# Kernel tuning notes

Measured on AMD Instinct MI355X. Metric: run time of the kernel, lower is better.

## Reference

```python
import jax, jax.numpy as jnp
import numpy as np

D_MODEL = 1024
NHEAD = 16
D_K = D_MODEL // NHEAD


def setup_inputs() -> dict:
    key = jax.random.key(0)
    ks = jax.random.split(key, 8)
    B, S, D = 4, 2048, D_MODEL
    scale = 1.0 / np.sqrt(D)  # rough xavier-like scale for weights
    return {
        "query": jax.random.normal(ks[0], (B, S, D), jnp.float32),
        "key_": jax.random.normal(ks[1], (B, S, D), jnp.float32),
        "value": jax.random.normal(ks[2], (B, S, D), jnp.float32),
        "w_q": jax.random.normal(ks[3], (D, D), jnp.float32) * scale,
        "w_k": jax.random.normal(ks[4], (D, D), jnp.float32) * scale,
        "w_v": jax.random.normal(ks[5], (D, D), jnp.float32) * scale,
        "w_o": jax.random.normal(ks[6], (D, D), jnp.float32) * scale,
        "b_o": jnp.zeros((D,), jnp.float32),
    }


def reference(query, key_, value, w_q, w_k, w_v, w_o, b_o):
    B, S, D = query.shape
    H, dk = NHEAD, D_K
    # torch Linear: x @ W.T ; reshape to [B, H, S, dk]
    def split_heads(x, w):
        return (x @ w.T).reshape(B, S, H, dk).transpose(0, 2, 1, 3)

    Q = split_heads(query, w_q)
    K = split_heads(key_, w_k)
    V = split_heads(value, w_v)

    scores = jnp.einsum("bhqd,bhkd->bhqk", Q, K) / jnp.sqrt(jnp.float32(dk))
    attn = jax.nn.softmax(scores, axis=-1)  # [B,H,S,S]
    ctx = jnp.einsum("bhqk,bhkd->bhqd", attn, V)
    ctx = ctx.transpose(0, 2, 1, 3).reshape(B, S, D)
    out = ctx @ w_o.T + b_o
    return out
```

## Files before the change

kernel.cpp:

```cpp
#include <hip/hip_runtime.h>
#include <hip/hip_bf16.h>
#include <stdint.h>

#define D_MODEL 1024
#define NHEAD   16
#define DK      64
#define BATCH   4
#define SEQ     2048
#define MROWS   (BATCH*SEQ)

typedef __hip_bfloat16 bf16;
typedef __attribute__((ext_vector_type(8))) short short8;
typedef __attribute__((ext_vector_type(4))) float f32x4;
typedef __attribute__((ext_vector_type(4))) unsigned int uint4t;

typedef __attribute__((address_space(1))) unsigned int as1_uint;
typedef __attribute__((address_space(3))) unsigned int as3_uint;

#define MFMA32(a,b,c) __builtin_amdgcn_mfma_f32_16x16x32_bf16((a),(b),(c),0,0,0)

static __device__ __forceinline__ void load_lds16(const bf16* g, bf16* l) {
  __builtin_amdgcn_global_load_lds((const as1_uint*)g, (as3_uint*)l, 16, 0, 0);
}

static __device__ __forceinline__ unsigned short bfbits(float x) {
  __hip_bfloat16 h = __float2bfloat16(x);
  return __builtin_bit_cast(unsigned short, h);
}

static __device__ __forceinline__ unsigned int pack2(float lo, float hi) {
  return (unsigned int)bfbits(lo) | ((unsigned int)bfbits(hi) << 16);
}

static __device__ __forceinline__ unsigned int pack2t(float lo, float hi) {
  return (__builtin_bit_cast(unsigned int, lo) >> 16) |
         (__builtin_bit_cast(unsigned int, hi) & 0xffff0000u);
}

__global__ __launch_bounds__(256) void cast_w(const float* __restrict__ i0,
                                              const float* __restrict__ i1,
                                              const float* __restrict__ i2,
                                              const float* __restrict__ i3,
                                              bf16* o0, bf16* o1, bf16* o2, bf16* o3,
                                              float s1) {
  const int z = blockIdx.z;
  const float* in = z == 0 ? i0 : (z == 1 ? i1 : (z == 2 ? i2 : i3));
  bf16* out = z == 0 ? o0 : (z == 1 ? o1 : (z == 2 ? o2 : o3));
  const float s = (z == 1) ? s1 : 1.0f;
  int i = blockIdx.x * 256 + threadIdx.x;
  const float4* p = (const float4*)in;
  float4 a = p[2 * (size_t)i];
  float4 b = p[2 * (size_t)i + 1];
  uint4t u;
  u.x = pack2(a.x * s, a.y * s);
  u.y = pack2(a.z * s, a.w * s);
  u.z = pack2(b.x * s, b.y * s);
  u.w = pack2(b.z * s, b.w * s);
  *(uint4t*)(out + (size_t)i * 8) = u;
}

__global__ __launch_bounds__(256) void cast_x(const float* __restrict__ i0,
                                              const float* __restrict__ i1,
                                              const float* __restrict__ i2,
                                              bf16* o0, bf16* o1, bf16* o2) {
  const int z = blockIdx.z;
  const float* in = z == 0 ? i0 : (z == 1 ? i1 : i2);
  bf16* out = z == 0 ? o0 : (z == 1 ? o1 : o2);
  int i = blockIdx.x * 256 + threadIdx.x;
  const float4* p = (const float4*)in;
  float4 a = p[2 * (size_t)i];
  float4 b = p[2 * (size_t)i + 1];
  uint4t u;
  u.x = pack2(a.x, a.y);
  u.y = pack2(a.z, a.w);
  u.z = pack2(b.x, b.y);
  u.w = pack2(b.z, b.w);
  *(uint4t*)(out + (size_t)i * 8) = u;
}

#define GEMM_STAGE(BUFOFF, KT) do {                                   \
    load_lds16(Ag0 + (KT), As + (BUFOFF) + w * 512);                  \
    load_lds16(Ag1 + (KT), As + (BUFOFF) + 2048 + w * 512);           \
    load_lds16(Bg0 + (KT), Bs + (BUFOFF) + w * 512);                  \
    load_lds16(Bg1 + (KT), Bs + (BUFOFF) + 2048 + w * 512);           \
  } while (0)

#define GEMM_COMPUTE(BUFOFF) do {                                              \
    short8 af[4], bf_[4];                                                      \
    _Pragma("unroll") for (int i = 0; i < 4; ++i) {                            \
      af[i]  = *(const short8*)(As + (BUFOFF) + (wm + i * 16 + lm) * 32 + lq * 8); \
      bf_[i] = *(const short8*)(Bs + (BUFOFF) + (wn + i * 16 + lm) * 32 + lq * 8); \
    }                                                                          \
    _Pragma("unroll") for (int i = 0; i < 4; ++i)                              \
      _Pragma("unroll") for (int j = 0; j < 4; ++j)                            \
        acc[i][j] = MFMA32(af[i], bf_[j], acc[i][j]);                          \
  } while (0)

#define VMCNT0_BAR() do {                                   \
    asm volatile("s_waitcnt vmcnt(0)" ::: "memory");        \
    __syncthreads();                                        \
  } while (0)

__global__ __launch_bounds__(256) void gemm_proj(const bf16* __restrict__ A0,
                                                 const bf16* __restrict__ A1,
                                                 const bf16* __restrict__ A2,
                                                 const bf16* __restrict__ B0,
                                                 const bf16* __restrict__ B1,
                                                 const bf16* __restrict__ B2,
                                                 bf16* C0, bf16* C1, bf16* C2) {
  const int z = blockIdx.z;
  const bf16* A = z == 0 ? A0 : (z == 1 ? A1 : A2);
  const bf16* B = z == 0 ? B0 : (z == 1 ? B1 : B2);
  bf16* C = z == 0 ? C0 : (z == 1 ? C1 : C2);
  const int M = MROWS, N = D_MODEL, K = D_MODEL;

  __shared__ bf16 As[2 * 128 * 32];
  __shared__ bf16 Bs[2 * 128 * 32];
  const int t = threadIdx.x;
  const int w = t >> 6;
  const int lane = t & 63;
  const int lm = lane & 15;
  const int lq = lane >> 4;
  const int wm = (w >> 1) * 64;
  const int wn = (w & 1) * 64;
  const long rowA = (long)blockIdx.x * 128;
  const long rowB = (long)blockIdx.y * 128;

  const int srow = t >> 2;
  const int scol = (t & 3) * 8;
  const bf16* Ag0 = A + (rowA + srow) * K + scol;
  const bf16* Ag1 = A + (rowA + 64 + srow) * K + scol;
  const bf16* Bg0 = B + (rowB + srow) * K + scol;
  const bf16* Bg1 = B + (rowB + 64 + srow) * K + scol;

  const f32x4 fzero = {0.f, 0.f, 0.f, 0.f};
  f32x4 acc[4][4];
#pragma unroll
  for (int i = 0; i < 4; ++i)
#pragma unroll
    for (int j = 0; j < 4; ++j) acc[i][j] = fzero;

  GEMM_STAGE(0, 0);
  VMCNT0_BAR();
  for (int kt = 0; kt < K; kt += 64) {
    if (kt + 32 < K) GEMM_STAGE(4096, kt + 32);
    GEMM_COMPUTE(0);
    VMCNT0_BAR();
    if (kt + 64 < K) GEMM_STAGE(0, kt + 64);
    GEMM_COMPUTE(4096);
    VMCNT0_BAR();
  }

  if (z < 2) {
#pragma unroll
    for (int i = 0; i < 4; ++i) {
      long r0 = rowA + wm + i * 16 + lq * 4;
#pragma unroll
      for (int j = 0; j < 4; ++j) {
        long c = rowB + wn + j * 16 + lm;
#pragma unroll
        for (int r = 0; r < 4; ++r)
          C[(r0 + r) * N + c] = __float2bfloat16(acc[i][j][r]);
      }
    }
  } else {
#pragma unroll
    for (int j = 0; j < 4; ++j) {
      long c = rowB + wn + j * 16 + lm;
#pragma unroll
      for (int i = 0; i < 4; ++i) {
        long r0 = rowA + wm + i * 16 + lq * 4;
        long sp = (r0 & ~63L) | (((r0 >> 5) & 1) * 32) | ((r0 & 15) * 2) | ((r0 >> 4) & 1);
#pragma unroll
        for (int r = 0; r < 4; ++r)
          C[c * M + sp + r * 2] = __float2bfloat16(acc[i][j][r]);
      }
    }
  }
}

__global__ __launch_bounds__(256) void gemm_out(const bf16* __restrict__ A,
                                                const bf16* __restrict__ B,
                                                float* __restrict__ C,
                                                const float* __restrict__ bias) {
  const int M = MROWS, N = D_MODEL, K = D_MODEL;
  __shared__ bf16 As[2 * 128 * 32];
  __shared__ bf16 Bs[2 * 128 * 32];
  const int t = threadIdx.x;
  const int w = t >> 6;
  const int lane = t & 63;
  const int lm = lane & 15;
  const int lq = lane >> 4;
  const int wm = (w >> 1) * 64;
  const int wn = (w & 1) * 64;
  const long rowA = (long)blockIdx.x * 128;
  const long rowB = (long)blockIdx.y * 128;

  const int srow = t >> 2;
  const int scol = (t & 3) * 8;
  const bf16* Ag0 = A + (rowA + srow) * K + scol;
  const bf16* Ag1 = A + (rowA + 64 + srow) * K + scol;
  const bf16* Bg0 = B + (rowB + srow) * K + scol;
  const bf16* Bg1 = B + (rowB + 64 + srow) * K + scol;

  const f32x4 fzero = {0.f, 0.f, 0.f, 0.f};
  f32x4 acc[4][4];
#pragma unroll
  for (int i = 0; i < 4; ++i)
#pragma unroll
    for (int j = 0; j < 4; ++j) acc[i][j] = fzero;

  GEMM_STAGE(0, 0);
  VMCNT0_BAR();
  for (int kt = 0; kt < K; kt += 64) {
    if (kt + 32 < K) GEMM_STAGE(4096, kt + 32);
    GEMM_COMPUTE(0);
    VMCNT0_BAR();
    if (kt + 64 < K) GEMM_STAGE(0, kt + 64);
    GEMM_COMPUTE(4096);
    VMCNT0_BAR();
  }

#pragma unroll
  for (int j = 0; j < 4; ++j) {
    long c = rowB + wn + j * 16 + lm;
    float bz = bias[c];
#pragma unroll
    for (int i = 0; i < 4; ++i) {
      long r0 = rowA + wm + i * 16 + lq * 4;
#pragma unroll
      for (int r = 0; r < 4; ++r)
        C[(r0 + r) * N + c] = acc[i][j][r] + bz;
    }
  }
}

__global__ __launch_bounds__(256, 4) void attn_kernel(const bf16* __restrict__ Qb,
                                                      const bf16* __restrict__ Kb,
                                                      const bf16* __restrict__ Vt,
                                                      bf16* __restrict__ ctx) {
  __shared__ bf16 Ks[64 * 64];
  __shared__ bf16 Vs[64 * 64];
  const int t = threadIdx.x;
  const int w = t >> 6;
  const int lane = t & 63;
  const int lm = lane & 15;
  const int lq = lane >> 4;
  const int bh = blockIdx.x;
  const int b = bh >> 4;
  const int h = bh & 15;
  const int q0 = blockIdx.y * 128 + w * 32;

  const bf16* Qh = Qb + (long)b * SEQ * D_MODEL + h * DK;
  const bf16* Kh = Kb + (long)b * SEQ * D_MODEL + h * DK;
  const bf16* Vh = Vt + (long)h * DK * MROWS + (long)b * SEQ;

  const int sr = lane >> 3;
  const int sc = ((lane & 7) ^ sr) * 8;
  const bf16* kg0 = Kh + (long)(w * 8 + sr) * D_MODEL + sc;
  const bf16* kg1 = Kh + (long)(32 + w * 8 + sr) * D_MODEL + sc;
  const bf16* vg0 = Vh + (long)(w * 8 + sr) * MROWS + sc;
  const bf16* vg1 = Vh + (long)(32 + w * 8 + sr) * MROWS + sc;
  bf16* lk0 = Ks + w * 512;
  bf16* lk1 = Ks + 2048 + w * 512;
  bf16* lv0 = Vs + w * 512;
  bf16* lv1 = Vs + 2048 + w * 512;

  short8 qf[2][2];
#pragma unroll
  for (int qt = 0; qt < 2; ++qt)
#pragma unroll
    for (int ks = 0; ks < 2; ++ks)
      qf[qt][ks] = *(const short8*)(Qh + (long)(q0 + qt * 16 + lm) * D_MODEL + ks * 32 + lq * 8);

  uint4t uo;
  uo.x = 0x3F803F80u; uo.y = 0x3F803F80u; uo.z = 0x3F803F80u; uo.w = 0x3F803F80u;
  const short8 ones8 = __builtin_bit_cast(short8, uo);

  const f32x4 fzero = {0.f, 0.f, 0.f, 0.f};
  f32x4 O[2][4];
  f32x4 lsum[2];
#pragma unroll
  for (int qt = 0; qt < 2; ++qt) {
    lsum[qt] = fzero;
#pragma unroll
    for (int dt = 0; dt < 4; ++dt) O[qt][dt] = fzero;
  }

  const int xs = lm & 7;

  for (int kv = 0; kv < SEQ; kv += 64) {
    load_lds16(kg0, lk0);
    load_lds16(kg1, lk1);
    load_lds16(vg0, lv0);
    load_lds16(vg1, lv1);
    kg0 += 64 * D_MODEL; kg1 += 64 * D_MODEL;
    vg0 += 64; vg1 += 64;
    asm volatile("s_waitcnt vmcnt(0)" ::: "memory");
    __syncthreads();

    short8 kf[4][2];
#pragma unroll
    for (int c = 0; c < 4; ++c)
#pragma unroll
      for (int ks = 0; ks < 2; ++ks)
        kf[c][ks] = *(const short8*)(Ks + (c * 16 + lm) * 64 + (((ks * 4 + lq) ^ xs) * 8));
    short8 vf[4][2];
#pragma unroll
    for (int dt = 0; dt < 4; ++dt)
#pragma unroll
      for (int tt = 0; tt < 2; ++tt)
        vf[dt][tt] = *(const short8*)(Vs + (dt * 16 + lm) * 64 + (((tt * 4 + lq) ^ xs) * 8));

#pragma unroll
    for (int qt = 0; qt < 2; ++qt) {
      f32x4 st[4];
#pragma unroll
      for (int c = 0; c < 4; ++c)
        st[c] = MFMA32(kf[c][0], qf[qt][0], fzero);
#pragma unroll
      for (int c = 0; c < 4; ++c)
        st[c] = MFMA32(kf[c][1], qf[qt][1], st[c]);

      float pe[4][4];
#pragma unroll
      for (int c = 0; c < 4; ++c)
#pragma unroll
        for (int r = 0; r < 4; ++r)
          pe[c][r] = __builtin_amdgcn_exp2f(st[c][r]);

      short8 pf8[2];
#pragma unroll
      for (int tt = 0; tt < 2; ++tt) {
        uint4t u;
        u.x = pack2t(pe[2 * tt][0], pe[2 * tt + 1][0]);
        u.y = pack2t(pe[2 * tt][1], pe[2 * tt + 1][1]);
        u.z = pack2t(pe[2 * tt][2], pe[2 * tt + 1][2]);
        u.w = pack2t(pe[2 * tt][3], pe[2 * tt + 1][3]);
        pf8[tt] = __builtin_bit_cast(short8, u);
      }

#pragma unroll
      for (int tt = 0; tt < 2; ++tt) {
        lsum[qt] = MFMA32(pf8[tt], ones8, lsum[qt]);
#pragma unroll
        for (int dt = 0; dt < 4; ++dt)
          O[qt][dt] = MFMA32(pf8[tt], vf[dt][tt], O[qt][dt]);
      }
    }
    __syncthreads();
  }

#pragma unroll
  for (int qt = 0; qt < 2; ++qt) {
    f32x4 linv;
#pragma unroll
    for (int r = 0; r < 4; ++r) linv[r] = 1.f / lsum[qt][r];
#pragma unroll
    for (int r = 0; r < 4; ++r) {
      long qrow = (long)b * SEQ + q0 + qt * 16 + lq * 4 + r;
#pragma unroll
      for (int dt = 0; dt < 4; ++dt)
        ctx[qrow * D_MODEL + h * DK + dt * 16 + lm] =
            __float2bfloat16(O[qt][dt][r] * linv[r]);
    }
  }
}

extern "C" void kernel_launch(void* const* d_in, const int* in_sizes, int n_in,
                              void* d_out, int out_size, void* d_ws, size_t ws_size,
                              hipStream_t stream) {
  const float* q  = (const float*)d_in[0];
  const float* k  = (const float*)d_in[1];
  const float* v  = (const float*)d_in[2];
  const float* wq = (const float*)d_in[3];
  const float* wk = (const float*)d_in[4];
  const float* wv = (const float*)d_in[5];
  const float* wo = (const float*)d_in[6];
  const float* bo = (const float*)d_in[7];

  char* ws = (char*)d_ws;
  const size_t SZW = (size_t)D_MODEL * D_MODEL * sizeof(bf16);
  const size_t SZX = (size_t)MROWS * D_MODEL * sizeof(bf16);
  bf16* Wq = (bf16*)(ws + 0 * SZW);
  bf16* Wk = (bf16*)(ws + 1 * SZW);
  bf16* Wv = (bf16*)(ws + 2 * SZW);
  bf16* Wo = (bf16*)(ws + 3 * SZW);
  bf16* Xq = (bf16*)(ws + 4 * SZW + 0 * SZX);
  bf16* Xk = (bf16*)(ws + 4 * SZW + 1 * SZX);
  bf16* Xv = (bf16*)(ws + 4 * SZW + 2 * SZX);
  bf16* Qb = (bf16*)(ws + 4 * SZW + 3 * SZX);
  bf16* Kb = (bf16*)(ws + 4 * SZW + 4 * SZX);
  bf16* Vt = Xq;
  bf16* Cx = Xk;

  const float SCL = 0.18033688011112042f;
  const int NW8 = D_MODEL * D_MODEL / 8;
  const int NX8 = MROWS * D_MODEL / 8;

  cast_w<<<dim3(NW8 / 256, 1, 4), 256, 0, stream>>>(wq, wk, wv, wo, Wq, Wk, Wv, Wo, SCL);
  cast_x<<<dim3(NX8 / 256, 1, 3), 256, 0, stream>>>(q, k, v, Xq, Xk, Xv);

  gemm_proj<<<dim3(MROWS / 128, D_MODEL / 128, 3), 256, 0, stream>>>(
      Xq, Xk, Xv, Wq, Wk, Wv, Qb, Kb, Vt);

  attn_kernel<<<dim3(BATCH * NHEAD, SEQ / 128), 256, 0, stream>>>(Qb, Kb, Vt, Cx);

  gemm_out<<<dim3(MROWS / 128, D_MODEL / 128), 256, 0, stream>>>(Cx, Wo, (float*)d_out, bo);
}
```

Measured before the change: 326.4 us.

## Fuse fp32-to-bf16 input cast into projection GEMM and double-buffer attention K/V

```diff
diff --git a/kernel.cpp b/kernel.cpp
--- a/kernel.cpp
+++ b/kernel.cpp
@@ -30,6 +30,12 @@
 
 static __device__ __forceinline__ unsigned int pack2(float lo, float hi) {
   return (unsigned int)bfbits(lo) | ((unsigned int)bfbits(hi) << 16);
+}
+
+static __device__ __forceinline__ unsigned int cvtpk(float lo, float hi) {
+  unsigned int d;
+  asm("v_cvt_pk_bf16_f32 %0, %1, %2" : "=v"(d) : "v"(lo), "v"(hi));
+  return d;
 }
 
 static __device__ __forceinline__ unsigned int pack2t(float lo, float hi) {
@@ -59,25 +65,6 @@
   *(uint4t*)(out + (size_t)i * 8) = u;
 }
 
-__global__ __launch_bounds__(256) void cast_x(const float* __restrict__ i0,
-                                              const float* __restrict__ i1,
-                                              const float* __restrict__ i2,
-                                              bf16* o0, bf16* o1, bf16* o2) {
-  const int z = blockIdx.z;
-  const float* in = z == 0 ? i0 : (z == 1 ? i1 : i2);
-  bf16* out = z == 0 ? o0 : (z == 1 ? o1 : o2);
-  int i = blockIdx.x * 256 + threadIdx.x;
-  const float4* p = (const float4*)in;
-  float4 a = p[2 * (size_t)i];
-  float4 b = p[2 * (size_t)i + 1];
-  uint4t u;
-  u.x = pack2(a.x, a.y);
-  u.y = pack2(a.z, a.w);
-  u.z = pack2(b.x, b.y);
-  u.w = pack2(b.z, b.w);
-  *(uint4t*)(out + (size_t)i * 8) = u;
-}
-
 #define GEMM_STAGE(BUFOFF, KT) do {                                   \
     load_lds16(Ag0 + (KT), As + (BUFOFF) + w * 512);                  \
     load_lds16(Ag1 + (KT), As + (BUFOFF) + 2048 + w * 512);           \
@@ -101,15 +88,37 @@
     __syncthreads();                                        \
   } while (0)
 
-__global__ __launch_bounds__(256) void gemm_proj(const bf16* __restrict__ A0,
-                                                 const bf16* __restrict__ A1,
-                                                 const bf16* __restrict__ A2,
+#define PROJ_LOADA(KT) do {                                  \
+    ar0 = *(const float4*)(Af0 + (KT));                      \
+    ar1 = *(const float4*)(Af0 + (KT) + 4);                  \
+    ar2 = *(const float4*)(Af1 + (KT));                      \
+    ar3 = *(const float4*)(Af1 + (KT) + 4);                  \
+  } while (0)
+
+#define PROJ_STOREA(BUFOFF) do {                             \
+    uint4t u0, u1;                                           \
+    u0.x = cvtpk(ar0.x, ar0.y); u0.y = cvtpk(ar0.z, ar0.w);  \
+    u0.z = cvtpk(ar1.x, ar1.y); u0.w = cvtpk(ar1.z, ar1.w);  \
+    u1.x = cvtpk(ar2.x, ar2.y); u1.y = cvtpk(ar2.z, ar2.w);  \
+    u1.z = cvtpk(ar3.x, ar3.y); u1.w = cvtpk(ar3.z, ar3.w);  \
+    *(uint4t*)(As + (BUFOFF) + t * 8) = u0;                  \
+    *(uint4t*)(As + (BUFOFF) + 2048 + t * 8) = u1;           \
+  } while (0)
+
+#define PROJ_STAGEB(BUFOFF, KT) do {                                  \
+    load_lds16(Bg0 + (KT), Bs + (BUFOFF) + w * 512);                  \
+    load_lds16(Bg1 + (KT), Bs + (BUFOFF) + 2048 + w * 512);           \
+  } while (0)
+
+__global__ __launch_bounds__(256) void gemm_proj(const float* __restrict__ A0,
+                                                 const float* __restrict__ A1,
+                                                 const float* __restrict__ A2,
                                                  const bf16* __restrict__ B0,
                                                  const bf16* __restrict__ B1,
                                                  const bf16* __restrict__ B2,
                                                  bf16* C0, bf16* C1, bf16* C2) {
   const int z = blockIdx.z;
-  const bf16* A = z == 0 ? A0 : (z == 1 ? A1 : A2);
+  const float* A = z == 0 ? A0 : (z == 1 ? A1 : A2);
   const bf16* B = z == 0 ? B0 : (z == 1 ? B1 : B2);
   bf16* C = z == 0 ? C0 : (z == 1 ? C1 : C2);
   const int M = MROWS, N = D_MODEL, K = D_MODEL;
@@ -128,11 +137,13 @@
 
   const int srow = t >> 2;
   const int scol = (t & 3) * 8;
-  const bf16* Ag0 = A + (rowA + srow) * K + scol;
-  const bf16* Ag1 = A + (rowA + 64 + srow) * K + scol;
+  const float* Af0 = A + (rowA + srow) * K + scol;
+  const float* Af1 = A + (rowA + 64 + srow) * K + scol;
   const bf16* Bg0 = B + (rowB + srow) * K + scol;
   const bf16* Bg1 = B + (rowB + 64 + srow) * K + scol;
 
+  float4 ar0, ar1, ar2, ar3;
+
   const f32x4 fzero = {0.f, 0.f, 0.f, 0.f};
   f32x4 acc[4][4];
 #pragma unroll
@@ -140,15 +151,21 @@
 #pragma unroll
     for (int j = 0; j < 4; ++j) acc[i][j] = fzero;
 
-  GEMM_STAGE(0, 0);
+  PROJ_LOADA(0);
+  PROJ_STAGEB(0, 0);
+  PROJ_STOREA(0);
   VMCNT0_BAR();
   for (int kt = 0; kt < K; kt += 64) {
-    if (kt + 32 < K) GEMM_STAGE(4096, kt + 32);
+    if (kt + 32 < K) { PROJ_LOADA(kt + 32); PROJ_STAGEB(4096, kt + 32); }
     GEMM_COMPUTE(0);
-    VMCNT0_BAR();
-    if (kt + 64 < K) GEMM_STAGE(0, kt + 64);
+    asm volatile("s_waitcnt vmcnt(0)" ::: "memory");
+    if (kt + 32 < K) PROJ_STOREA(4096);
+    __syncthreads();
+    if (kt + 64 < K) { PROJ_LOADA(kt + 64); PROJ_STAGEB(0, kt + 64); }
     GEMM_COMPUTE(4096);
-    VMCNT0_BAR();
+    asm volatile("s_waitcnt vmcnt(0)" ::: "memory");
+    if (kt + 64 < K) PROJ_STOREA(0);
+    __syncthreads();
   }
 
   if (z < 2) {
@@ -235,12 +252,57 @@
   }
 }
 
+#define ATTN_STAGE(BUF) do {                                 \
+    load_lds16(kg0, Ks + (BUF) + w * 512);                   \
+    load_lds16(kg1, Ks + (BUF) + 2048 + w * 512);            \
+    load_lds16(vg0, Vs + (BUF) + w * 512);                   \
+    load_lds16(vg1, Vs + (BUF) + 2048 + w * 512);            \
+    kg0 += 64 * D_MODEL; kg1 += 64 * D_MODEL;                \
+    vg0 += 64; vg1 += 64;                                    \
+  } while (0)
+
+#define ATTN_COMPUTE(BUF) do {                                                       \
+    short8 kf[4][2];                                                                 \
+    _Pragma("unroll") for (int c = 0; c < 4; ++c)                                    \
+      _Pragma("unroll") for (int ks = 0; ks < 2; ++ks)                               \
+        kf[c][ks] = *(const short8*)(Ks + (BUF) + (c * 16 + lm) * 64 + (((ks * 4 + lq) ^ xs) * 8)); \
+    short8 vf[4][2];                                                                 \
+    _Pragma("unroll") for (int dt = 0; dt < 4; ++dt)                                 \
+      _Pragma("unroll") for (int tt = 0; tt < 2; ++tt)                               \
+        vf[dt][tt] = *(const short8*)(Vs + (BUF) + (dt * 16 + lm) * 64 + (((tt * 4 + lq) ^ xs) * 8)); \
+    _Pragma("unroll") for (int qt = 0; qt < 2; ++qt) {                               \
+      f32x4 st[4];                                                                   \
+      _Pragma("unroll") for (int c = 0; c < 4; ++c)                                  \
+        st[c] = MFMA32(kf[c][0], qf[qt][0], fzero);                                  \
+      _Pragma("unroll") for (int c = 0; c < 4; ++c)                                  \
+        st[c] = MFMA32(kf[c][1], qf[qt][1], st[c]);                                  \
+      float pe[4][4];                                                                \
+      _Pragma("unroll") for (int c = 0; c < 4; ++c)                                  \
+        _Pragma("unroll") for (int r = 0; r < 4; ++r)                                \
+          pe[c][r] = __builtin_amdgcn_exp2f(st[c][r]);                               \
+      short8 pf8[2];                                                                 \
+      _Pragma("unroll") for (int tt = 0; tt < 2; ++tt) {                             \
+        uint4t u;                                                                    \
+        u.x = pack2t(pe[2 * tt][0], pe[2 * tt + 1][0]);                              \
+        u.y = pack2t(pe[2 * tt][1], pe[2 * tt + 1][1]);                              \
+        u.z = pack2t(pe[2 * tt][2], pe[2 * tt + 1][2]);                              \
+        u.w = pack2t(pe[2 * tt][3], pe[2 * tt + 1][3]);                              \
+        pf8[tt] = __builtin_bit_cast(short8, u);                                     \
+      }                                                                              \
+      _Pragma("unroll") for (int tt = 0; tt < 2; ++tt) {                             \
+        lsum[qt] = MFMA32(pf8[tt], ones8, lsum[qt]);                                 \
+        _Pragma("unroll") for (int dt = 0; dt < 4; ++dt)                             \
+          O[qt][dt] = MFMA32(pf8[tt], vf[dt][tt], O[qt][dt]);                        \
+      }                                                                              \
+    }                                                                                \
+  } while (0)
+
 __global__ __launch_bounds__(256, 4) void attn_kernel(const bf16* __restrict__ Qb,
                                                       const bf16* __restrict__ Kb,
                                                       const bf16* __restrict__ Vt,
                                                       bf16* __restrict__ ctx) {
-  __shared__ bf16 Ks[64 * 64];
-  __shared__ bf16 Vs[64 * 64];
+  __shared__ bf16 Ks[2 * 64 * 64];
+  __shared__ bf16 Vs[2 * 64 * 64];
   const int t = threadIdx.x;
   const int w = t >> 6;
   const int lane = t & 63;
@@ -261,10 +323,6 @@
   const bf16* kg1 = Kh + (long)(32 + w * 8 + sr) * D_MODEL + sc;
   const bf16* vg0 = Vh + (long)(w * 8 + sr) * MROWS + sc;
   const bf16* vg1 = Vh + (long)(32 + w * 8 + sr) * MROWS + sc;
-  bf16* lk0 = Ks + w * 512;
-  bf16* lk1 = Ks + 2048 + w * 512;
-  bf16* lv0 = Vs + w * 512;
-  bf16* lv1 = Vs + 2048 + w * 512;
 
   short8 qf[2][2];
 #pragma unroll
@@ -289,66 +347,15 @@
 
   const int xs = lm & 7;
 
-  for (int kv = 0; kv < SEQ; kv += 64) {
-    load_lds16(kg0, lk0);
-    load_lds16(kg1, lk1);
-    load_lds16(vg0, lv0);
-    load_lds16(vg1, lv1);
-    kg0 += 64 * D_MODEL; kg1 += 64 * D_MODEL;
-    vg0 += 64; vg1 += 64;
-    asm volatile("s_waitcnt vmcnt(0)" ::: "memory");
-    __syncthreads();
-
-    short8 kf[4][2];
-#pragma unroll
-    for (int c = 0; c < 4; ++c)
-#pragma unroll
-      for (int ks = 0; ks < 2; ++ks)
-        kf[c][ks] = *(const short8*)(Ks + (c * 16 + lm) * 64 + (((ks * 4 + lq) ^ xs) * 8));
-    short8 vf[4][2];
-#pragma unroll
-    for (int dt = 0; dt < 4; ++dt)
-#pragma unroll
-      for (int tt = 0; tt < 2; ++tt)
-        vf[dt][tt] = *(const short8*)(Vs + (dt * 16 + lm) * 64 + (((tt * 4 + lq) ^ xs) * 8));
-
-#pragma unroll
-    for (int qt = 0; qt < 2; ++qt) {
-      f32x4 st[4];
-#pragma unroll
-      for (int c = 0; c < 4; ++c)
-        st[c] = MFMA32(kf[c][0], qf[qt][0], fzero);
-#pragma unroll
-      for (int c = 0; c < 4; ++c)
-        st[c] = MFMA32(kf[c][1], qf[qt][1], st[c]);
-
-      float pe[4][4];
-#pragma unroll
-      for (int c = 0; c < 4; ++c)
-#pragma unroll
-        for (int r = 0; r < 4; ++r)
-          pe[c][r] = __builtin_amdgcn_exp2f(st[c][r]);
-
-      short8 pf8[2];
-#pragma unroll
-      for (int tt = 0; tt < 2; ++tt) {
-        uint4t u;
-        u.x = pack2t(pe[2 * tt][0], pe[2 * tt + 1][0]);
-        u.y = pack2t(pe[2 * tt][1], pe[2 * tt + 1][1]);
-        u.z = pack2t(pe[2 * tt][2], pe[2 * tt + 1][2]);
-        u.w = pack2t(pe[2 * tt][3], pe[2 * tt + 1][3]);
-        pf8[tt] = __builtin_bit_cast(short8, u);
-      }
-
-#pragma unroll
-      for (int tt = 0; tt < 2; ++tt) {
-        lsum[qt] = MFMA32(pf8[tt], ones8, lsum[qt]);
-#pragma unroll
-        for (int dt = 0; dt < 4; ++dt)
-          O[qt][dt] = MFMA32(pf8[tt], vf[dt][tt], O[qt][dt]);
-      }
-    }
-    __syncthreads();
+  ATTN_STAGE(0);
+  VMCNT0_BAR();
+  for (int kv = 0; kv < SEQ; kv += 128) {
+    if (kv + 64 < SEQ) ATTN_STAGE(4096);
+    ATTN_COMPUTE(0);
+    VMCNT0_BAR();
+    if (kv + 128 < SEQ) ATTN_STAGE(0);
+    ATTN_COMPUTE(4096);
+    VMCNT0_BAR();
   }
 
 #pragma unroll
@@ -386,23 +393,18 @@
   bf16* Wk = (bf16*)(ws + 1 * SZW);
   bf16* Wv = (bf16*)(ws + 2 * SZW);
   bf16* Wo = (bf16*)(ws + 3 * SZW);
-  bf16* Xq = (bf16*)(ws + 4 * SZW + 0 * SZX);
-  bf16* Xk = (bf16*)(ws + 4 * SZW + 1 * SZX);
-  bf16* Xv = (bf16*)(ws + 4 * SZW + 2 * SZX);
+  bf16* Vt = (bf16*)(ws + 4 * SZW + 0 * SZX);
+  bf16* Cx = (bf16*)(ws + 4 * SZW + 1 * SZX);
   bf16* Qb = (bf16*)(ws + 4 * SZW + 3 * SZX);
   bf16* Kb = (bf16*)(ws + 4 * SZW + 4 * SZX);
-  bf16* Vt = Xq;
-  bf16* Cx = Xk;
 
   const float SCL = 0.18033688011112042f;
   const int NW8 = D_MODEL * D_MODEL / 8;
-  const int NX8 = MROWS * D_MODEL / 8;
 
   cast_w<<<dim3(NW8 / 256, 1, 4), 256, 0, stream>>>(wq, wk, wv, wo, Wq, Wk, Wv, Wo, SCL);
-  cast_x<<<dim3(NX8 / 256, 1, 3), 256, 0, stream>>>(q, k, v, Xq, Xk, Xv);
 
   gemm_proj<<<dim3(MROWS / 128, D_MODEL / 128, 3), 256, 0, stream>>>(
-      Xq, Xk, Xv, Wq, Wk, Wv, Qb, Kb, Vt);
+      q, k, v, Wq, Wk, Wv, Qb, Kb, Vt);
 
   attn_kernel<<<dim3(BATCH * NHEAD, SEQ / 128), 256, 0, stream>>>(Qb, Kb, Vt, Cx);
 
```

After: 410.1 us. 1.26x slower.
